# Optimization experiments

Hardware: AMD Instinct MI355X
Metric: run time of the kernel (lower is better)

The kernel has to match this reference:

```python
import jax, jax.numpy as jnp
import numpy as np

L, D, H, DH, WS, FF = 4, 256, 8, 32, 128, 1024
B, N = 2, 8192
SCALE = DH ** -0.5
EPS = 1e-8


def setup_inputs() -> dict:
    key = jax.random.key(0)
    ks = jax.random.split(key, 24)
    nrm = lambda k, shape, s=0.02: jax.random.normal(k, shape, dtype=jnp.float32) * s
    d = {}
    d["x_real"] = jax.random.normal(ks[0], (B, N, D), dtype=jnp.float32)
    d["x_imag"] = jax.random.normal(ks[1], (B, N, D), dtype=jnp.float32)
    # complex attention projection weights, stored [in, out] (y = x @ W)
    d["Wq_r"] = nrm(ks[2], (L, D, D)); d["Wq_i"] = nrm(ks[3], (L, D, D))
    d["Wk_r"] = nrm(ks[4], (L, D, D)); d["Wk_i"] = nrm(ks[5], (L, D, D))
    d["Wv_r"] = nrm(ks[6], (L, D, D)); d["Wv_i"] = nrm(ks[7], (L, D, D))
    d["Wo_r"] = nrm(ks[8], (L, D, D)); d["Wo_i"] = nrm(ks[9], (L, D, D))
    d["rel_bias"] = nrm(ks[10], (L, 2 * WS + 1))  # std=0.02 per nn.init.normal_
    d["norm1_scale"] = jnp.ones((L, D), jnp.float32)
    d["norm2_scale"] = jnp.ones((L, D), jnp.float32)
    # ComplexFeedForward: real nn.Linear pairs with biases
    d["W1_r"] = nrm(ks[11], (L, D, FF)); d["b1_r"] = jnp.zeros((L, FF), jnp.float32)
    d["W1_i"] = nrm(ks[12], (L, D, FF)); d["b1_i"] = jnp.zeros((L, FF), jnp.float32)
    d["W2_r"] = nrm(ks[13], (L, FF, D)); d["b2_r"] = jnp.zeros((L, D), jnp.float32)
    d["W2_i"] = nrm(ks[14], (L, FF, D)); d["b2_i"] = jnp.zeros((L, D), jnp.float32)
    return d


def _rmsnorm(xr, xi, scale):
    rms = jnp.sqrt(jnp.mean(xr * xr + xi * xi, axis=-1, keepdims=True) + EPS)
    return xr / rms * scale, xi / rms * scale


def _cmm(xr, xi, Wr, Wi):
    # (xr + i xi) @ (Wr + i Wi)
    return xr @ Wr - xi @ Wi, xr @ Wi + xi @ Wr


def _split_heads(t):  # [B,N,H*DH] -> [B,H,NW,WS,DH]
    return t.reshape(B, N // WS, WS, H, DH).transpose(0, 3, 1, 2, 4)


def _attn(xr, xi, Wq_r, Wq_i, Wk_r, Wk_i, Wv_r, Wv_i, Wo_r, Wo_i, rel_bias):
    qr, qi = _cmm(xr, xi, Wq_r, Wq_i)
    kr, ki = _cmm(xr, xi, Wk_r, Wk_i)
    vr, vi = _cmm(xr, xi, Wv_r, Wv_i)
    qr, qi, kr, ki, vr, vi = map(_split_heads, (qr, qi, kr, ki, vr, vi))
    # Re(q . conj(k)) = qr.kr + qi.ki ; windowed (N % WS == 0, no padding)
    dots = (jnp.einsum('bhwid,bhwjd->bhwij', qr, kr)
            + jnp.einsum('bhwid,bhwjd->bhwij', qi, ki)) * SCALE
    idx = (jnp.arange(WS)[None, :] - jnp.arange(WS)[:, None]).clip(-WS, WS) + WS
    dots = dots + rel_bias[idx]  # broadcast over b,h,w
    attn = jax.nn.softmax(dots, axis=-1)  # real-valued probs
    or_ = jnp.einsum('bhwij,bhwjd->bhwid', attn, vr)
    oi_ = jnp.einsum('bhwij,bhwjd->bhwid', attn, vi)
    merge = lambda t: t.transpose(0, 2, 3, 1, 4).reshape(B, N, H * DH)
    or_, oi_ = merge(or_), merge(oi_)
    return _cmm(or_, oi_, Wo_r, Wo_i)


def _ffn(xr, xi, W1_r, b1_r, W1_i, b1_i, W2_r, b2_r, W2_i, b2_i):
    # faithful: w_real(x.real) - w_imag(x.imag) etc., each linear carries its bias
    hr = (xr @ W1_r + b1_r) - (xi @ W1_i + b1_i)
    hi = (xi @ W1_r + b1_r) + (xr @ W1_i + b1_i)
    hr = jax.nn.gelu(hr, approximate=False)
    hi = jax.nn.gelu(hi, approximate=False)
    yr = (hr @ W2_r + b2_r) - (hi @ W2_i + b2_i)
    yi = (hi @ W2_r + b2_r) + (hr @ W2_i + b2_i)
    return yr, yi


def _forward(x_real, x_imag, Wq_r, Wq_i, Wk_r, Wk_i, Wv_r, Wv_i, Wo_r, Wo_i,
             rel_bias, norm1_scale, norm2_scale,
             W1_r, b1_r, W1_i, b1_i, W2_r, b2_r, W2_i, b2_i):
    xr, xi = x_real, x_imag
    for l in range(L):
        nr, ni = _rmsnorm(xr, xi, norm1_scale[l])
        ar, ai = _attn(nr, ni, Wq_r[l], Wq_i[l], Wk_r[l], Wk_i[l],
                       Wv_r[l], Wv_i[l], Wo_r[l], Wo_i[l], rel_bias[l])
        xr, xi = xr + ar, xi + ai
        nr, ni = _rmsnorm(xr, xi, norm2_scale[l])
        fr, fi = _ffn(nr, ni, W1_r[l], b1_r[l], W1_i[l], b1_i[l],
                      W2_r[l], b2_r[l], W2_i[l], b2_i[l])
        xr, xi = xr + fr, xi + fi
    return jnp.stack([xr, xi])  # [2, B, N, D]


def reference(x_real, x_imag, Wq_r, Wq_i, Wk_r, Wk_i, Wv_r, Wv_i, Wo_r, Wo_i,
              rel_bias, norm1_scale, norm2_scale,
              W1_r, b1_r, W1_i, b1_i, W2_r, b2_r, W2_i, b2_i):
    return _forward(x_real, x_imag, Wq_r, Wq_i, Wk_r, Wk_i, Wv_r, Wv_i,
                    Wo_r, Wo_i, rel_bias, norm1_scale, norm2_scale,
                    W1_r, b1_r, W1_i, b1_i, W2_r, b2_r, W2_i, b2_i)
```

## Files before the change

kernel.cpp:

```cpp
#include <hip/hip_runtime.h>
#include <cstdint>


typedef __bf16 bf16x8 __attribute__((ext_vector_type(8)));
typedef float  f32x4  __attribute__((ext_vector_type(4)));

#define M_TOK 16384
#define LDX   512

__device__ __forceinline__ unsigned short f2bf(float f) {
    union { float f; unsigned int u; } v; v.f = f;
    unsigned int r = v.u + 0x7FFFu + ((v.u >> 16) & 1u);
    return (unsigned short)(r >> 16);
}

__device__ __forceinline__ void async16(const void* g, void* l) {
    __builtin_amdgcn_global_load_lds(
        (const __attribute__((address_space(1))) void*)g,
        (__attribute__((address_space(3))) void*)l, 16, 0, 0);
}


__global__ __launch_bounds__(256) void copyin_kernel(const float* __restrict__ xr,
                                                     const float* __restrict__ xi,
                                                     float* __restrict__ X) {
    int idx = blockIdx.x * 256 + threadIdx.x;
    int t = idx >> 7, c4 = idx & 127;
    float4 v = (c4 < 64) ? ((const float4*)xr)[t * 64 + c4]
                         : ((const float4*)xi)[t * 64 + (c4 - 64)];
    ((float4*)X)[idx] = v;
}

__global__ __launch_bounds__(256) void unpack_kernel(const float* __restrict__ X,
                                                     float* __restrict__ out) {
    int idx = blockIdx.x * 256 + threadIdx.x;
    int p = idx >> 20;
    int rem = idx & 1048575;
    int t = rem >> 6, d4 = rem & 63;
    ((float4*)out)[idx] = ((const float4*)X)[t * 128 + p * 64 + d4];
}


__global__ __launch_bounds__(256) void pack_qkv_kernel(
    const float* __restrict__ Wq_r, const float* __restrict__ Wq_i,
    const float* __restrict__ Wk_r, const float* __restrict__ Wk_i,
    const float* __restrict__ Wv_r, const float* __restrict__ Wv_i,
    unsigned short* __restrict__ out) {
    int idx = blockIdx.x * 256 + threadIdx.x;
    int l = idx / 786432;
    int rem = idx - l * 786432;
    int n = rem >> 9, k = rem & 511;
    int blk = n >> 8;
    int no = n & 255, kk = k & 255;
    bool khi = (k >= 256);
    bool imag = (blk & 1);
    const float *Wr, *Wi;
    int proj = blk >> 1;
    if (proj == 0)      { Wr = Wq_r; Wi = Wq_i; }
    else if (proj == 1) { Wr = Wk_r; Wi = Wk_i; }
    else                { Wr = Wv_r; Wi = Wv_i; }
    int wi = l * 65536 + kk * 256 + no;
    float val = !imag ? (khi ? -Wi[wi] : Wr[wi])
                      : (khi ?  Wr[wi] : Wi[wi]);
    out[idx] = f2bf(val);
}

__global__ __launch_bounds__(256) void pack_o_kernel(
    const float* __restrict__ Wo_r, const float* __restrict__ Wo_i,
    unsigned short* __restrict__ out) {
    int idx = blockIdx.x * 256 + threadIdx.x;
    int l = idx >> 18;
    int rem = idx & 262143;
    int n = rem >> 9, k = rem & 511;
    bool imag = (n >= 256);
    int no = n & 255, kk = k & 255;
    bool khi = (k >= 256);
    int wi = l * 65536 + kk * 256 + no;
    float val = !imag ? (khi ? -Wo_i[wi] : Wo_r[wi])
                      : (khi ?  Wo_r[wi] : Wo_i[wi]);
    out[idx] = f2bf(val);
}

__global__ __launch_bounds__(256) void pack_ffn1_kernel(
    const float* __restrict__ W1_r, const float* __restrict__ W1_i,
    unsigned short* __restrict__ out) {
    int idx = blockIdx.x * 256 + threadIdx.x;
    int l = idx >> 20;
    int rem = idx & 1048575;
    int n = rem >> 9, k = rem & 511;
    bool imag = (n >= 1024);
    int no = imag ? n - 1024 : n;
    int kk = k & 255;
    bool khi = (k >= 256);
    int wi = l * 262144 + kk * 1024 + no;
    float val = !imag ? (khi ? -W1_i[wi] : W1_r[wi])
                      : (khi ?  W1_r[wi] : W1_i[wi]);
    out[idx] = f2bf(val);
}

__global__ __launch_bounds__(256) void pack_ffn2_kernel(
    const float* __restrict__ W2_r, const float* __restrict__ W2_i,
    unsigned short* __restrict__ out) {
    int idx = blockIdx.x * 256 + threadIdx.x;
    int l = idx >> 20;
    int rem = idx & 1048575;
    int n = rem >> 11, k = rem & 2047;
    bool imag = (n >= 256);
    int no = n & 255;
    int kk = k & 1023;
    bool khi = (k >= 1024);
    int wi = l * 262144 + kk * 256 + no;
    float val = !imag ? (khi ? -W2_i[wi] : W2_r[wi])
                      : (khi ?  W2_r[wi] : W2_i[wi]);
    out[idx] = f2bf(val);
}

__global__ __launch_bounds__(256) void pack_bias_kernel(
    const float* __restrict__ b1r, const float* __restrict__ b1i,
    const float* __restrict__ b2r, const float* __restrict__ b2i,
    float* __restrict__ B1, float* __restrict__ B2) {
    int idx = blockIdx.x * 256 + threadIdx.x;
    if (idx < 8192) {
        int l = idx >> 11, n = idx & 2047;
        bool imag = (n >= 1024);
        int no = imag ? n - 1024 : n;
        int bi = l * 1024 + no;
        B1[idx] = imag ? (b1r[bi] + b1i[bi]) : (b1r[bi] - b1i[bi]);
    } else {
        int i2 = idx - 8192;
        int l = i2 >> 9, n = i2 & 511;
        bool imag = (n >= 256);
        int no = n & 255;
        int bi = l * 256 + no;
        B2[i2] = imag ? (b2r[bi] + b2i[bi]) : (b2r[bi] - b2i[bi]);
    }
}


__global__ __launch_bounds__(256) void rmsnorm_kernel(const float* __restrict__ X,
                                                      const float* __restrict__ scale,
                                                      unsigned short* __restrict__ out) {
    int row = blockIdx.x * 4 + (threadIdx.x >> 6);
    int lane = threadIdx.x & 63;
    const float4* xrow = (const float4*)(X + (size_t)row * LDX);
    float4 xr = xrow[lane];
    float4 xi = xrow[64 + lane];
    float ss = xr.x * xr.x + xr.y * xr.y + xr.z * xr.z + xr.w * xr.w
             + xi.x * xi.x + xi.y * xi.y + xi.z * xi.z + xi.w * xi.w;
#pragma unroll
    for (int m = 1; m < 64; m <<= 1) ss += __shfl_xor(ss, m);
    float inv = 1.0f / sqrtf(ss * (1.0f / 256.0f) + 1e-8f);
    float4 sc = ((const float4*)scale)[lane];
    ushort4 o0, o1;
    o0.x = f2bf(xr.x * inv * sc.x); o0.y = f2bf(xr.y * inv * sc.y);
    o0.z = f2bf(xr.z * inv * sc.z); o0.w = f2bf(xr.w * inv * sc.w);
    o1.x = f2bf(xi.x * inv * sc.x); o1.y = f2bf(xi.y * inv * sc.y);
    o1.z = f2bf(xi.z * inv * sc.z); o1.w = f2bf(xi.w * inv * sc.w);
    ushort4* orow = (ushort4*)(out + (size_t)row * LDX);
    orow[lane] = o0;
    orow[64 + lane] = o1;
}


template <int MODE>
__global__ __launch_bounds__(256) void gemm_kernel(
    const unsigned short* __restrict__ A, const unsigned short* __restrict__ Bt,
    unsigned short* __restrict__ Obf, const float* __restrict__ bias,
    float* __restrict__ Xres, int K, int N) {
    __shared__ __align__(16) char smem[32768];
    char* sA = smem;
    char* sB = smem + 16384;
    const int tid = threadIdx.x;
    const int lane = tid & 63;
    const int wave = tid >> 6;
    const int g = lane >> 4;
    const int rl = lane & 15;
    const int wm = wave >> 1, wn = wave & 1;
    const int tM = blockIdx.y, tN = blockIdx.x;

    f32x4 acc[4][4];
#pragma unroll
    for (int i = 0; i < 4; ++i)
#pragma unroll
        for (int j = 0; j < 4; ++j)
#pragma unroll
            for (int v = 0; v < 4; ++v) acc[i][j][v] = 0.0f;

    const unsigned short* Abase = A + (size_t)tM * 128 * K;
    const unsigned short* Bbase = Bt + (size_t)tN * 128 * K;

    for (int kt = 0; kt < K; kt += 64) {
#pragma unroll
        for (int it = 0; it < 4; ++it) {
            int s = it * 256 + tid;
            int r = s >> 3;
            int c = (s & 7) ^ (r & 7);
            async16(Abase + (size_t)r * K + kt + c * 8, sA + (it * 256 + wave * 64) * 16);
            async16(Bbase + (size_t)r * K + kt + c * 8, sB + (it * 256 + wave * 64) * 16);
        }
        asm volatile("s_waitcnt vmcnt(0)" ::: "memory");
        __syncthreads();
#pragma unroll
        for (int ks = 0; ks < 2; ++ks) {
            bf16x8 aF[4], bF[4];
#pragma unroll
            for (int fm = 0; fm < 4; ++fm) {
                int r = wm * 64 + fm * 16 + rl;
                int c = ks * 4 + g;
                aF[fm] = *(const bf16x8*)(sA + r * 128 + ((c ^ (r & 7)) << 4));
            }
#pragma unroll
            for (int fn = 0; fn < 4; ++fn) {
                int r = wn * 64 + fn * 16 + rl;
                int c = ks * 4 + g;
                bF[fn] = *(const bf16x8*)(sB + r * 128 + ((c ^ (r & 7)) << 4));
            }
#pragma unroll
            for (int fm = 0; fm < 4; ++fm)
#pragma unroll
                for (int fn = 0; fn < 4; ++fn)
                    acc[fm][fn] = __builtin_amdgcn_mfma_f32_16x16x32_bf16(
                        aF[fm], bF[fn], acc[fm][fn], 0, 0, 0);
        }
        __syncthreads();
    }

#pragma unroll
    for (int fm = 0; fm < 4; ++fm)
#pragma unroll
        for (int fn = 0; fn < 4; ++fn)
#pragma unroll
            for (int v = 0; v < 4; ++v) {
                int row = tM * 128 + wm * 64 + fm * 16 + g * 4 + v;
                int col = tN * 128 + wn * 64 + fn * 16 + rl;
                float val = acc[fm][fn][v];
                if (MODE == 0) {
                    Obf[(size_t)row * N + col] = f2bf(val);
                } else if (MODE == 1) {
                    float x = val + bias[col];
                    float ge = 0.5f * x * (1.0f + erff(x * 0.70710678118654752f));
                    Obf[(size_t)row * N + col] = f2bf(ge);
                } else {
                    float x = val + (bias ? bias[col] : 0.0f);
                    Xres[(size_t)row * LDX + col] += x;
                }
            }
}


#define AT_KOFF 16384
#define AT_VOFF 34816
#define AT_ROFF 52224

__global__ __launch_bounds__(256) void attn_kernel(
    const unsigned short* __restrict__ qkv, const float* __restrict__ relb_g,
    unsigned short* __restrict__ attout) {
    __shared__ __align__(16) char smem[53264];
    const int tid = threadIdx.x;
    const int lane = tid & 63;
    const int wq = tid >> 6;
    const int g = lane >> 4;
    const int rl = lane & 15;
    const int w = blockIdx.x, h = blockIdx.y, b = blockIdx.z;
    const int tok0 = b * 8192 + w * 128;
    float* relb = (float*)(smem + AT_ROFF);

    for (int i = tid; i < 257; i += 256) relb[i] = relb_g[i];

#pragma unroll
    for (int it = 0; it < 4; ++it) {
        int s = it * 256 + tid;
        int r = s >> 3;
        int c = (s & 7) ^ (r & 7);
        int colq = (c < 4) ? (h * 32 + c * 8) : (256 + h * 32 + (c - 4) * 8);
        const unsigned short* rowp = qkv + (size_t)(tok0 + r) * 1536;
        *(float4*)(smem + s * 16) = *(const float4*)(rowp + colq);
        *(float4*)(smem + AT_KOFF + s * 16) = *(const float4*)(rowp + colq + 512);
    }
#pragma unroll
    for (int it = 0; it < 4; ++it) {
        int e = it * 256 + tid;
        int j = e >> 3;
        int d0 = (e & 7) * 8;
        int colv = (d0 < 32) ? (1024 + h * 32 + d0) : (1280 + h * 32 + (d0 - 32));
        float4 vv = *(const float4*)(qkv + (size_t)(tok0 + j) * 1536 + colv);
        const unsigned short* u = (const unsigned short*)&vv;
#pragma unroll
        for (int k = 0; k < 8; ++k)
            *(unsigned short*)(smem + AT_VOFF + ((d0 + k) * 136 + j) * 2) = u[k];
    }
    __syncthreads();

    f32x4 accS[2][8];
#pragma unroll
    for (int i = 0; i < 2; ++i)
#pragma unroll
        for (int j = 0; j < 8; ++j)
#pragma unroll
            for (int v = 0; v < 4; ++v) accS[i][j][v] = 0.0f;

#pragma unroll
    for (int ks = 0; ks < 2; ++ks) {
        bf16x8 qf[2], kf[8];
        int c = ks * 4 + g;
#pragma unroll
        for (int fm = 0; fm < 2; ++fm) {
            int r = wq * 32 + fm * 16 + rl;
            qf[fm] = *(const bf16x8*)(smem + r * 128 + ((c ^ (r & 7)) << 4));
        }
#pragma unroll
        for (int fn = 0; fn < 8; ++fn) {
            int r = fn * 16 + rl;
            kf[fn] = *(const bf16x8*)(smem + AT_KOFF + r * 128 + ((c ^ (r & 7)) << 4));
        }
#pragma unroll
        for (int fm = 0; fm < 2; ++fm)
#pragma unroll
            for (int fn = 0; fn < 8; ++fn)
                accS[fm][fn] = __builtin_amdgcn_mfma_f32_16x16x32_bf16(
                    qf[fm], kf[fn], accS[fm][fn], 0, 0, 0);
    }

#pragma unroll
    for (int fm = 0; fm < 2; ++fm)
#pragma unroll
        for (int v = 0; v < 4; ++v) {
            int i = wq * 32 + fm * 16 + g * 4 + v;
            float m = -1e30f;
#pragma unroll
            for (int fn = 0; fn < 8; ++fn) {
                int j = fn * 16 + rl;
                float s = accS[fm][fn][v] * 0.17677669529663687f + relb[j - i + 128];
                accS[fm][fn][v] = s;
                m = fmaxf(m, s);
            }
            m = fmaxf(m, __shfl_xor(m, 1));
            m = fmaxf(m, __shfl_xor(m, 2));
            m = fmaxf(m, __shfl_xor(m, 4));
            m = fmaxf(m, __shfl_xor(m, 8));
            float sum = 0.0f;
#pragma unroll
            for (int fn = 0; fn < 8; ++fn) {
                float p = __expf(accS[fm][fn][v] - m);
                accS[fm][fn][v] = p;
                sum += p;
            }
            sum += __shfl_xor(sum, 1);
            sum += __shfl_xor(sum, 2);
            sum += __shfl_xor(sum, 4);
            sum += __shfl_xor(sum, 8);
            float inv = 1.0f / sum;
#pragma unroll
            for (int fn = 0; fn < 8; ++fn) accS[fm][fn][v] *= inv;
        }

    __syncthreads();

#pragma unroll
    for (int fm = 0; fm < 2; ++fm)
#pragma unroll
        for (int fn = 0; fn < 8; ++fn)
#pragma unroll
            for (int v = 0; v < 4; ++v) {
                int i = wq * 32 + fm * 16 + g * 4 + v;
                int j = fn * 16 + rl;
                ((unsigned short*)smem)[i * 136 + j] = f2bf(accS[fm][fn][v]);
            }
    __syncthreads();

    f32x4 accO[2][4];
#pragma unroll
    for (int i = 0; i < 2; ++i)
#pragma unroll
        for (int j = 0; j < 4; ++j)
#pragma unroll
            for (int v = 0; v < 4; ++v) accO[i][j][v] = 0.0f;

#pragma unroll
    for (int ks = 0; ks < 4; ++ks) {
        bf16x8 pf[2], vf[4];
#pragma unroll
        for (int fm = 0; fm < 2; ++fm) {
            int r = wq * 32 + fm * 16 + rl;
            pf[fm] = *(const bf16x8*)(smem + r * 272 + ks * 64 + g * 16);
        }
#pragma unroll
        for (int fn = 0; fn < 4; ++fn) {
            int n = fn * 16 + rl;
            vf[fn] = *(const bf16x8*)(smem + AT_VOFF + n * 272 + ks * 64 + g * 16);
        }
#pragma unroll
        for (int fm = 0; fm < 2; ++fm)
#pragma unroll
            for (int fn = 0; fn < 4; ++fn)
                accO[fm][fn] = __builtin_amdgcn_mfma_f32_16x16x32_bf16(
                    pf[fm], vf[fn], accO[fm][fn], 0, 0, 0);
    }

#pragma unroll
    for (int fm = 0; fm < 2; ++fm)
#pragma unroll
        for (int fn = 0; fn < 4; ++fn)
#pragma unroll
            for (int v = 0; v < 4; ++v) {
                int i = wq * 32 + fm * 16 + g * 4 + v;
                int dc = fn * 16 + rl;
                int col = (dc < 32) ? (h * 32 + dc) : (256 + h * 32 + (dc - 32));
                attout[(size_t)(tok0 + i) * 512 + col] = f2bf(accO[fm][fn][v]);
            }
}


extern "C" void kernel_launch(void* const* d_in, const int* in_sizes, int n_in,
                              void* d_out, int out_size, void* d_ws, size_t ws_size,
                              hipStream_t stream) {
    const float* x_real = (const float*)d_in[0];
    const float* x_imag = (const float*)d_in[1];
    const float* Wq_r = (const float*)d_in[2];
    const float* Wq_i = (const float*)d_in[3];
    const float* Wk_r = (const float*)d_in[4];
    const float* Wk_i = (const float*)d_in[5];
    const float* Wv_r = (const float*)d_in[6];
    const float* Wv_i = (const float*)d_in[7];
    const float* Wo_r = (const float*)d_in[8];
    const float* Wo_i = (const float*)d_in[9];
    const float* rel_bias = (const float*)d_in[10];
    const float* norm1 = (const float*)d_in[11];
    const float* norm2 = (const float*)d_in[12];
    const float* W1_r = (const float*)d_in[13];
    const float* b1_r = (const float*)d_in[14];
    const float* W1_i = (const float*)d_in[15];
    const float* b1_i = (const float*)d_in[16];
    const float* W2_r = (const float*)d_in[17];
    const float* b2_r = (const float*)d_in[18];
    const float* W2_i = (const float*)d_in[19];
    const float* b2_i = (const float*)d_in[20];

    char* ws = (char*)d_ws;
    float*          X    = (float*)(ws + 0);
    unsigned short* NRM  = (unsigned short*)(ws + 33554432);
    unsigned short* QKVH = (unsigned short*)(ws + 50331648);
    unsigned short* ATTO = (unsigned short*)(ws + 117440512);
    unsigned short* WQKV = (unsigned short*)(ws + 134217728);
    unsigned short* WO   = (unsigned short*)(ws + 140509184);
    unsigned short* W1P  = (unsigned short*)(ws + 142606336);
    unsigned short* W2P  = (unsigned short*)(ws + 150994944);
    float*          B1   = (float*)(ws + 159383552);
    float*          B2   = (float*)(ws + 159416320);

    copyin_kernel<<<8192, 256, 0, stream>>>(x_real, x_imag, X);
    pack_qkv_kernel<<<12288, 256, 0, stream>>>(Wq_r, Wq_i, Wk_r, Wk_i, Wv_r, Wv_i, WQKV);
    pack_o_kernel<<<4096, 256, 0, stream>>>(Wo_r, Wo_i, WO);
    pack_ffn1_kernel<<<16384, 256, 0, stream>>>(W1_r, W1_i, W1P);
    pack_ffn2_kernel<<<16384, 256, 0, stream>>>(W2_r, W2_i, W2P);
    pack_bias_kernel<<<40, 256, 0, stream>>>(b1_r, b1_i, b2_r, b2_i, B1, B2);

    for (int l = 0; l < 4; ++l) {
        rmsnorm_kernel<<<4096, 256, 0, stream>>>(X, norm1 + l * 256, NRM);
        gemm_kernel<0><<<dim3(12, 128), 256, 0, stream>>>(
            NRM, WQKV + (size_t)l * 786432, QKVH, nullptr, nullptr, 512, 1536);
        attn_kernel<<<dim3(64, 8, 2), 256, 0, stream>>>(QKVH, rel_bias + l * 257, ATTO);
        gemm_kernel<2><<<dim3(4, 128), 256, 0, stream>>>(
            ATTO, WO + (size_t)l * 262144, nullptr, nullptr, X, 512, 512);
        rmsnorm_kernel<<<4096, 256, 0, stream>>>(X, norm2 + l * 256, NRM);
        gemm_kernel<1><<<dim3(16, 128), 256, 0, stream>>>(
            NRM, W1P + (size_t)l * 1048576, QKVH, B1 + l * 2048, nullptr, 512, 2048);
        gemm_kernel<2><<<dim3(4, 128), 256, 0, stream>>>(
            QKVH, W2P + (size_t)l * 1048576, nullptr, B2 + l * 512, X, 2048, 512);
    }
    unpack_kernel<<<8192, 256, 0, stream>>>(X, (float*)d_out);
}
```

Measured before the change: 1.100 ms.

## Replace GEMM with 8-wave double-buffered ping-pong kernel using larger tiles

Replaces the single-buffered 128x128, 4-wave GEMM with a 512-thread kernel that computes a 256xBN tile (BN of 128 or 256) in four quadrants. Async global-to-LDS loads for upcoming K tiles are interleaved between quadrant MFMA phases, with partial vmcnt waits, barriers and s_setprio. The aim is to hide global memory latency behind MFMA work and raise operand reuse per block. In exchange the kernel uses much more LDS and registers (one block per CU), launches fewer blocks, and depends on a fragile hand-tuned waitcnt schedule.

```diff
diff --git a/kernel.cpp b/kernel.cpp
--- a/kernel.cpp
+++ b/kernel.cpp
@@ -162,89 +162,154 @@
 }
 
 
-template <int MODE>
-__global__ __launch_bounds__(256) void gemm_kernel(
+template <int BN, int MODE>
+__global__ __launch_bounds__(512, 1) void gemm8_kernel(
     const unsigned short* __restrict__ A, const unsigned short* __restrict__ Bt,
     unsigned short* __restrict__ Obf, const float* __restrict__ bias,
     float* __restrict__ Xres, int K, int N) {
-    __shared__ __align__(16) char smem[32768];
-    char* sA = smem;
-    char* sB = smem + 16384;
+    constexpr int FN = BN / 128;
+    constexpr int HB = BN * 64;
+    constexpr int LB = BN / 128;
+    __shared__ __align__(16) char smem[65536 + 4 * HB];
     const int tid = threadIdx.x;
     const int lane = tid & 63;
     const int wave = tid >> 6;
-    const int g = lane >> 4;
-    const int rl = lane & 15;
-    const int wm = wave >> 1, wn = wave & 1;
+    const int g = lane >> 4, rl = lane & 15;
+    const int wm = wave >> 2, wn = wave & 3;
     const int tM = blockIdx.y, tN = blockIdx.x;
-
-    f32x4 acc[4][4];
-#pragma unroll
-    for (int i = 0; i < 4; ++i)
-#pragma unroll
-        for (int j = 0; j < 4; ++j)
-#pragma unroll
-            for (int v = 0; v < 4; ++v) acc[i][j][v] = 0.0f;
-
-    const unsigned short* Abase = A + (size_t)tM * 128 * K;
-    const unsigned short* Bbase = Bt + (size_t)tN * 128 * K;
-
-    for (int kt = 0; kt < K; kt += 64) {
-#pragma unroll
-        for (int it = 0; it < 4; ++it) {
-            int s = it * 256 + tid;
-            int r = s >> 3;
-            int c = (s & 7) ^ (r & 7);
-            async16(Abase + (size_t)r * K + kt + c * 8, sA + (it * 256 + wave * 64) * 16);
-            async16(Bbase + (size_t)r * K + kt + c * 8, sB + (it * 256 + wave * 64) * 16);
-        }
-        asm volatile("s_waitcnt vmcnt(0)" ::: "memory");
-        __syncthreads();
-#pragma unroll
-        for (int ks = 0; ks < 2; ++ks) {
-            bf16x8 aF[4], bF[4];
-#pragma unroll
-            for (int fm = 0; fm < 4; ++fm) {
-                int r = wm * 64 + fm * 16 + rl;
-                int c = ks * 4 + g;
-                aF[fm] = *(const bf16x8*)(sA + r * 128 + ((c ^ (r & 7)) << 4));
-            }
-#pragma unroll
-            for (int fn = 0; fn < 4; ++fn) {
-                int r = wn * 64 + fn * 16 + rl;
-                int c = ks * 4 + g;
-                bF[fn] = *(const bf16x8*)(sB + r * 128 + ((c ^ (r & 7)) << 4));
-            }
+    const int NT = K >> 6, NTM = NT - 1, NIT = NT >> 1;
+
+    auto stageA = [&](int t, int mh) {
+        int tt = t & NTM;
+        const unsigned short* src = A + ((size_t)(tM * 256 + mh * 128)) * K + tt * 64;
+        char* dst = smem + ((tt & 1) * 2 + mh) * 16384;
+#pragma unroll
+        for (int it = 0; it < 2; ++it) {
+            int s = it * 512 + tid;
+            int r = s >> 3, c = (s & 7) ^ (r & 7);
+            async16(src + (size_t)r * K + c * 8, dst + (it * 512 + wave * 64) * 16);
+        }
+    };
+    auto stageB = [&](int t, int nh) {
+        int tt = t & NTM;
+        const unsigned short* src = Bt + ((size_t)(tN * BN + nh * (BN / 2))) * K + tt * 64;
+        char* dst = smem + 65536 + ((tt & 1) * 2 + nh) * HB;
+#pragma unroll
+        for (int it = 0; it < LB; ++it) {
+            int s = it * 512 + tid;
+            int r = s >> 3, c = (s & 7) ^ (r & 7);
+            async16(src + (size_t)r * K + c * 8, dst + (it * 512 + wave * 64) * 16);
+        }
+    };
+
+    f32x4 acc[2][2][4][FN];
+#pragma unroll
+    for (int a = 0; a < 2; ++a)
+#pragma unroll
+        for (int b = 0; b < 2; ++b)
+#pragma unroll
+            for (int c = 0; c < 4; ++c)
+#pragma unroll
+                for (int d = 0; d < FN; ++d)
+#pragma unroll
+                    for (int v = 0; v < 4; ++v) acc[a][b][c][d][v] = 0.0f;
+
+    bf16x8 aF[4][2], bF[FN][2];
+
+    stageA(0, 0); stageA(0, 1); stageB(0, 0); stageB(0, 1);
+    stageA(1, 0); stageB(1, 1); stageA(1, 1);
+    if constexpr (BN == 256) asm volatile("s_waitcnt vmcnt(6)" ::: "memory");
+    else                     asm volatile("s_waitcnt vmcnt(5)" ::: "memory");
+    __builtin_amdgcn_s_barrier();
+
+    for (int i = 0; i < NIT; ++i) {
+        const int t0 = 2 * i;
+#pragma unroll
+        for (int p = 0; p < 8; ++p) {
+            const int q = p & 3;
+            const int tt = t0 + (p >> 2);
+            const int b = tt & 1;
+            const int mh = q >> 1;
+            const int nh = (q == 1 || q == 2) ? 1 : 0;
+            if (q == 0 || q == 2) {
+                char* base = smem + (b * 2 + mh) * 16384;
+#pragma unroll
+                for (int fm = 0; fm < 4; ++fm) {
+                    int hr = wm * 64 + fm * 16 + rl;
+#pragma unroll
+                    for (int ks = 0; ks < 2; ++ks) {
+                        int c = ks * 4 + g;
+                        aF[fm][ks] = *(const bf16x8*)(base + hr * 128 + ((c ^ (hr & 7)) << 4));
+                    }
+                }
+            }
+            if (q != 2) {
+                char* base = smem + 65536 + (b * 2 + nh) * HB;
+#pragma unroll
+                for (int fn = 0; fn < FN; ++fn) {
+                    int hr = wn * (FN * 16) + fn * 16 + rl;
+#pragma unroll
+                    for (int ks = 0; ks < 2; ++ks) {
+                        int c = ks * 4 + g;
+                        bF[fn][ks] = *(const bf16x8*)(base + hr * 128 + ((c ^ (hr & 7)) << 4));
+                    }
+                }
+            }
+            switch (p) {
+                case 0: stageB(t0 + 1, 0); break;
+                case 1: stageA(t0 + 2, 0); break;
+                case 2: stageB(t0 + 2, 1); break;
+                case 3: stageA(t0 + 2, 1); break;
+                case 4: stageB(t0 + 2, 0); break;
+                case 5: stageA(t0 + 3, 0); break;
+                case 6: stageB(t0 + 3, 1); break;
+                case 7: stageA(t0 + 3, 1); break;
+            }
+            __builtin_amdgcn_s_barrier();
+            asm volatile("s_waitcnt lgkmcnt(0)" ::: "memory");
+            __builtin_amdgcn_s_setprio(1);
 #pragma unroll
             for (int fm = 0; fm < 4; ++fm)
 #pragma unroll
-                for (int fn = 0; fn < 4; ++fn)
-                    acc[fm][fn] = __builtin_amdgcn_mfma_f32_16x16x32_bf16(
-                        aF[fm], bF[fn], acc[fm][fn], 0, 0, 0);
-        }
-        __syncthreads();
-    }
-
-#pragma unroll
-    for (int fm = 0; fm < 4; ++fm)
-#pragma unroll
-        for (int fn = 0; fn < 4; ++fn)
-#pragma unroll
-            for (int v = 0; v < 4; ++v) {
-                int row = tM * 128 + wm * 64 + fm * 16 + g * 4 + v;
-                int col = tN * 128 + wn * 64 + fn * 16 + rl;
-                float val = acc[fm][fn][v];
-                if (MODE == 0) {
-                    Obf[(size_t)row * N + col] = f2bf(val);
-                } else if (MODE == 1) {
-                    float x = val + bias[col];
-                    float ge = 0.5f * x * (1.0f + erff(x * 0.70710678118654752f));
-                    Obf[(size_t)row * N + col] = f2bf(ge);
-                } else {
-                    float x = val + (bias ? bias[col] : 0.0f);
-                    Xres[(size_t)row * LDX + col] += x;
-                }
-            }
+                for (int fn = 0; fn < FN; ++fn)
+#pragma unroll
+                    for (int ks = 0; ks < 2; ++ks)
+                        acc[mh][nh][fm][fn] = __builtin_amdgcn_mfma_f32_16x16x32_bf16(
+                            aF[fm][ks], bF[fn][ks], acc[mh][nh][fm][fn], 0, 0, 0);
+            __builtin_amdgcn_s_setprio(0);
+            if (q == 3) {
+                if constexpr (BN == 256) asm volatile("s_waitcnt vmcnt(6)" ::: "memory");
+                else                     asm volatile("s_waitcnt vmcnt(5)" ::: "memory");
+            }
+            __builtin_amdgcn_s_barrier();
+        }
+    }
+    asm volatile("s_waitcnt vmcnt(0)" ::: "memory");
+
+#pragma unroll
+    for (int mh = 0; mh < 2; ++mh)
+#pragma unroll
+        for (int nh = 0; nh < 2; ++nh)
+#pragma unroll
+            for (int fm = 0; fm < 4; ++fm)
+#pragma unroll
+                for (int fn = 0; fn < FN; ++fn)
+#pragma unroll
+                    for (int v = 0; v < 4; ++v) {
+                        int row = tM * 256 + mh * 128 + wm * 64 + fm * 16 + g * 4 + v;
+                        int col = tN * BN + nh * (BN / 2) + wn * (FN * 16) + fn * 16 + rl;
+                        float val = acc[mh][nh][fm][fn][v];
+                        if (MODE == 0) {
+                            Obf[(size_t)row * N + col] = f2bf(val);
+                        } else if (MODE == 1) {
+                            float x = val + bias[col];
+                            float ge = 0.5f * x * (1.0f + erff(x * 0.70710678118654752f));
+                            Obf[(size_t)row * N + col] = f2bf(ge);
+                        } else {
+                            float x = val + (bias ? bias[col] : 0.0f);
+                            Xres[(size_t)row * LDX + col] += x;
+                        }
+                    }
 }
 
 
@@ -457,15 +522,15 @@
 
     for (int l = 0; l < 4; ++l) {
         rmsnorm_kernel<<<4096, 256, 0, stream>>>(X, norm1 + l * 256, NRM);
-        gemm_kernel<0><<<dim3(12, 128), 256, 0, stream>>>(
+        gemm8_kernel<128, 0><<<dim3(12, 64), 512, 0, stream>>>(
             NRM, WQKV + (size_t)l * 786432, QKVH, nullptr, nullptr, 512, 1536);
         attn_kernel<<<dim3(64, 8, 2), 256, 0, stream>>>(QKVH, rel_bias + l * 257, ATTO);
-        gemm_kernel<2><<<dim3(4, 128), 256, 0, stream>>>(
+        gemm8_kernel<128, 2><<<dim3(4, 64), 512, 0, stream>>>(
             ATTO, WO + (size_t)l * 262144, nullptr, nullptr, X, 512, 512);
         rmsnorm_kernel<<<4096, 256, 0, stream>>>(X, norm2 + l * 256, NRM);
-        gemm_kernel<1><<<dim3(16, 128), 256, 0, stream>>>(
+        gemm8_kernel<256, 1><<<dim3(8, 64), 512, 0, stream>>>(
             NRM, W1P + (size_t)l * 1048576, QKVH, B1 + l * 2048, nullptr, 512, 2048);
-        gemm_kernel<2><<<dim3(4, 128), 256, 0, stream>>>(
+        gemm8_kernel<128, 2><<<dim3(4, 64), 512, 0, stream>>>(
             QKVH, W2P + (size_t)l * 1048576, nullptr, B2 + l * 512, X, 2048, 512);
     }
     unpack_kernel<<<8192, 256, 0, stream>>>(X, (float*)d_out);
```

Result: slower. 1.298 ms (+18.0%).

## Double-buffer GEMM LDS tiles and remap blocks across XCDs

Applied to the files above, without the earlier changes.

The GEMM kernel now uses two 32KB LDS buffers and issues the async global-to-LDS loads for the next K tile before computing on the current one, so memory latency can overlap with MFMA work. Launches switch to a 1D grid whose block index is remapped so consecutive tiles land on the same XCD, aiming for better L2 reuse of A and B tiles. The doubled LDS use (64KB) may lower occupancy. The loop relies on a single barrier per iteration and no explicit vmcnt wait before reading the next buffer, which may be a correctness risk.

```diff
diff --git a/kernel.cpp b/kernel.cpp
--- a/kernel.cpp
+++ b/kernel.cpp
@@ -166,40 +166,56 @@
 __global__ __launch_bounds__(256) void gemm_kernel(
     const unsigned short* __restrict__ A, const unsigned short* __restrict__ Bt,
     unsigned short* __restrict__ Obf, const float* __restrict__ bias,
-    float* __restrict__ Xres, int K, int N) {
-    __shared__ __align__(16) char smem[32768];
-    char* sA = smem;
-    char* sB = smem + 16384;
+    float* __restrict__ Xres, int K, int N, int nTn) {
+    __shared__ __align__(16) char smem[65536];
     const int tid = threadIdx.x;
     const int lane = tid & 63;
     const int wave = tid >> 6;
     const int g = lane >> 4;
     const int rl = lane & 15;
     const int wm = wave >> 1, wn = wave & 1;
-    const int tM = blockIdx.y, tN = blockIdx.x;
-
-    f32x4 acc[4][4];
-#pragma unroll
-    for (int i = 0; i < 4; ++i)
-#pragma unroll
-        for (int j = 0; j < 4; ++j)
-#pragma unroll
-            for (int v = 0; v < 4; ++v) acc[i][j][v] = 0.0f;
+
+    const int nwg = gridDim.x;
+    const int qs = nwg >> 3;
+    const int xcd = blockIdx.x & 7, pos = blockIdx.x >> 3;
+    const int wg = xcd * qs + pos;
+    const int tM = wg / nTn, tN = wg - tM * nTn;
 
     const unsigned short* Abase = A + (size_t)tM * 128 * K;
     const unsigned short* Bbase = Bt + (size_t)tN * 128 * K;
-
-    for (int kt = 0; kt < K; kt += 64) {
+    const int NT = K >> 6;
+
+    auto stage = [&](int t, int buf) {
+        char* dA = smem + buf * 32768;
+        char* dB = dA + 16384;
+        const unsigned short* As = Abase + t * 64;
+        const unsigned short* Bs = Bbase + t * 64;
 #pragma unroll
         for (int it = 0; it < 4; ++it) {
             int s = it * 256 + tid;
-            int r = s >> 3;
-            int c = (s & 7) ^ (r & 7);
-            async16(Abase + (size_t)r * K + kt + c * 8, sA + (it * 256 + wave * 64) * 16);
-            async16(Bbase + (size_t)r * K + kt + c * 8, sB + (it * 256 + wave * 64) * 16);
-        }
-        asm volatile("s_waitcnt vmcnt(0)" ::: "memory");
-        __syncthreads();
+            int r = s >> 3, c = (s & 7) ^ (r & 7);
+            async16(As + (size_t)r * K + c * 8, dA + (it * 256 + wave * 64) * 16);
+            async16(Bs + (size_t)r * K + c * 8, dB + (it * 256 + wave * 64) * 16);
+        }
+    };
+
+    f32x4 acc[4][4];
+#pragma unroll
+    for (int i = 0; i < 4; ++i)
+#pragma unroll
+        for (int j = 0; j < 4; ++j)
+#pragma unroll
+            for (int v = 0; v < 4; ++v) acc[i][j][v] = 0.0f;
+
+    stage(0, 0);
+    asm volatile("s_waitcnt vmcnt(0)" ::: "memory");
+    __syncthreads();
+
+    int cur = 0;
+    for (int t = 0; t < NT; ++t) {
+        if (t + 1 < NT) stage(t + 1, cur ^ 1);
+        char* sA = smem + cur * 32768;
+        char* sB = sA + 16384;
 #pragma unroll
         for (int ks = 0; ks < 2; ++ks) {
             bf16x8 aF[4], bF[4];
@@ -223,6 +239,7 @@
                         aF[fm], bF[fn], acc[fm][fn], 0, 0, 0);
         }
         __syncthreads();
+        cur ^= 1;
     }
 
 #pragma unroll
@@ -457,16 +474,16 @@
 
     for (int l = 0; l < 4; ++l) {
         rmsnorm_kernel<<<4096, 256, 0, stream>>>(X, norm1 + l * 256, NRM);
-        gemm_kernel<0><<<dim3(12, 128), 256, 0, stream>>>(
-            NRM, WQKV + (size_t)l * 786432, QKVH, nullptr, nullptr, 512, 1536);
+        gemm_kernel<0><<<1536, 256, 0, stream>>>(
+            NRM, WQKV + (size_t)l * 786432, QKVH, nullptr, nullptr, 512, 1536, 12);
         attn_kernel<<<dim3(64, 8, 2), 256, 0, stream>>>(QKVH, rel_bias + l * 257, ATTO);
-        gemm_kernel<2><<<dim3(4, 128), 256, 0, stream>>>(
-            ATTO, WO + (size_t)l * 262144, nullptr, nullptr, X, 512, 512);
+        gemm_kernel<2><<<512, 256, 0, stream>>>(
+            ATTO, WO + (size_t)l * 262144, nullptr, nullptr, X, 512, 512, 4);
         rmsnorm_kernel<<<4096, 256, 0, stream>>>(X, norm2 + l * 256, NRM);
-        gemm_kernel<1><<<dim3(16, 128), 256, 0, stream>>>(
-            NRM, W1P + (size_t)l * 1048576, QKVH, B1 + l * 2048, nullptr, 512, 2048);
-        gemm_kernel<2><<<dim3(4, 128), 256, 0, stream>>>(
-            QKVH, W2P + (size_t)l * 1048576, nullptr, B2 + l * 512, X, 2048, 512);
+        gemm_kernel<1><<<2048, 256, 0, stream>>>(
+            NRM, W1P + (size_t)l * 1048576, QKVH, B1 + l * 2048, nullptr, 512, 2048, 16);
+        gemm_kernel<2><<<512, 256, 0, stream>>>(
+            QKVH, W2P + (size_t)l * 1048576, nullptr, B2 + l * 512, X, 2048, 512, 4);
     }
     unpack_kernel<<<8192, 256, 0, stream>>>(X, (float*)d_out);
 }
```

Result: no change. 1.089 ms (-1.0%).
